# Kernel tuning notes

Measured on AMD Instinct MI355X. Metric: run time of the kernel, lower is better.

## Reference

```python
import jax, jax.numpy as jnp
import numpy as np

H8, W8 = 64, 64
H4, W4 = 128, 128
C_LAT, C_HI = 256, 128
N_Q = 1024
ORIG_H, ORIG_W = 512, 512
NUM_ITERS = 4
TEMP = 20.0
DIM = 4 + C_HI + C_LAT        # 388 mixer output dim
IN_DIM = DIM + 3 * 49         # 535 mixer input dim
HID = 512


def _unit(v):
    return v / jnp.sqrt(jnp.maximum(jnp.sum(v * v, axis=-1, keepdims=True), 1e-12))


def setup_inputs() -> dict:
    key = jax.random.key(0)
    ks = jax.random.split(key, 20)
    fg = _unit(jax.random.normal(ks[0], (1, H8, W8, C_LAT), jnp.float32))
    hg = _unit(jax.random.normal(ks[1], (1, H4, W4, C_HI), jnp.float32))
    qf = _unit(jax.random.normal(ks[2], (1, N_Q, C_LAT), jnp.float32))
    hq = _unit(jax.random.normal(ks[3], (1, N_Q, C_HI), jnp.float32))
    p = lambda k, s, sc=0.05: sc * jax.random.normal(k, s, jnp.float32)
    return dict(
        feature_grid=fg, hires_feats_grid=hg, query_feats=qf, hires_query_feats=hq,
        hid1_w=p(ks[4], (16, 1, 3, 3)), hid1_b=jnp.zeros((16,), jnp.float32),
        hid2_w=p(ks[5], (1, 16, 3, 3)), hid2_b=jnp.zeros((1,), jnp.float32),
        hid3_w=p(ks[6], (32, 16, 3, 3)), hid3_b=jnp.zeros((32,), jnp.float32),
        hid4_w=p(ks[7], (32, 16)), hid4_b=jnp.zeros((16,), jnp.float32),
        occ_w=p(ks[8], (16, 2)), occ_b=jnp.zeros((2,), jnp.float32),
        mix_in_w=p(ks[9], (IN_DIM, HID), 0.02), mix_in_b=jnp.zeros((HID,), jnp.float32),
        mix_out_w=p(ks[10], (HID, DIM), 0.02), mix_out_b=jnp.zeros((DIM,), jnp.float32),
    )


def _conv2d(x, w, b, stride, pad):
    y = jax.lax.conv_general_dilated(x, w, (stride, stride), pad,
                                     dimension_numbers=('NCHW', 'OIHW', 'NCHW'))
    return y + b[None, :, None, None]


def _bilinear_sample(grid, coords):
    # grid [H,W,C]; coords [..., 2] as (y, x); edge-clamped bilinear gather.
    H, W = grid.shape[0], grid.shape[1]
    y, x = coords[..., 0], coords[..., 1]
    y0f, x0f = jnp.floor(y), jnp.floor(x)
    wy, wx = (y - y0f)[..., None], (x - x0f)[..., None]
    y0 = jnp.clip(y0f.astype(jnp.int32), 0, H - 1)
    y1 = jnp.clip(y0f.astype(jnp.int32) + 1, 0, H - 1)
    x0 = jnp.clip(x0f.astype(jnp.int32), 0, W - 1)
    x1 = jnp.clip(x0f.astype(jnp.int32) + 1, 0, W - 1)
    g00, g01 = grid[y0, x0], grid[y0, x1]
    g10, g11 = grid[y1, x0], grid[y1, x1]
    return (g00 * (1 - wy) * (1 - wx) + g01 * (1 - wy) * wx
            + g10 * wy * (1 - wx) + g11 * wy * wx)


def _forward(fg, hg, qf, hq, hid1_w, hid1_b, hid2_w, hid2_b, hid3_w, hid3_b,
             hid4_w, hid4_b, occ_w, occ_b, mix_in_w, mix_in_b, mix_out_w, mix_out_b):
    # --- tracks_from_cost_volume ---
    cv = jnp.einsum('bnc,bhwc->bnhw', qf, fg)                 # [1,N,64,64]
    b, n, h, w = cv.shape
    x = cv.reshape(b * n, 1, h, w)
    occ_map = jax.nn.relu(_conv2d(x, hid1_w, hid1_b, 1, 'SAME'))   # [bn,16,h,w]
    pmap = _conv2d(occ_map, hid2_w, hid2_b, 1, 'SAME').reshape(b * n, h * w)
    heat = jax.nn.softmax(pmap * TEMP, axis=-1).reshape(b * n, h, w)
    ey = jnp.einsum('bhw,h->b', heat, jnp.arange(h, dtype=jnp.float32))
    ex = jnp.einsum('bhw,w->b', heat, jnp.arange(w, dtype=jnp.float32))
    points = jnp.stack([ex * (ORIG_W / w), ey * (ORIG_H / h)], -1).reshape(b, n, 2)
    op = jnp.pad(occ_map, ((0, 0), (0, 0), (0, 2), (0, 2)))
    o3 = jax.nn.relu(_conv2d(op, hid3_w, hid3_b, 2, 'VALID'))
    o3 = o3.mean((-1, -2))                                     # [bn,32]
    o3 = jax.nn.relu(o3 @ hid4_w + hid4_b)
    o3 = (o3 @ occ_w + occ_b).reshape(b, n, 2)
    occ, expd = o3[..., 0], o3[..., 1]

    # --- iterative pips refinement ---
    cy, cx = jnp.meshgrid(jnp.arange(-3, 4), jnp.arange(-3, 4), indexing='ij')
    ctx = jnp.stack([cy, cx], -1).reshape(-1, 2).astype(jnp.float32)   # [49,2] (dy,dx)
    fg_avg = fg.reshape(1, H8 // 2, 2, W8 // 2, 2, C_LAT).mean((2, 4))
    pyramid = [hg, fg, fg_avg]
    feats = jnp.concatenate([hq, qf], -1)                      # [1,N,384]
    pos = points
    for it in range(NUM_ITERS):
        if it == 0:
            queries = [hq[0], qf[0], qf[0]]
        else:
            queries = [feats[0, :, :C_HI], feats[0, :, C_HI:], feats[0, :, C_HI:]]
        corrs = []
        for grid, q in zip(pyramid, queries):
            gh, gw = grid.shape[1], grid.shape[2]
            scale = jnp.array([gw / ORIG_W, gh / ORIG_H], jnp.float32)
            c = (pos[0] * scale)[:, ::-1]                      # (x,y)->(y,x), [N,2]
            coords2 = c[:, None, :] + ctx[None]                # [N,49,2]
            nb = _bilinear_sample(grid[0], coords2)            # [N,49,C]
            corrs.append(jnp.einsum('nsc,nc->ns', nb, q))
        corrs = jnp.concatenate(corrs, -1)[None]               # [1,N,147]
        mlp_in = jnp.concatenate([jnp.zeros_like(pos), occ[..., None],
                                  expd[..., None], feats, corrs], -1)
        res = jax.nn.gelu(mlp_in @ mix_in_w + mix_in_b) @ mix_out_w + mix_out_b
        pos = pos + res[..., :2]
        occ = occ + res[..., 2]
        expd = expd + res[..., 3]
        feats = feats + res[..., 4:]
    return jnp.concatenate([pos, occ[..., None], expd[..., None]], -1)  # [1,N,4]


def reference(feature_grid, hires_feats_grid, query_feats, hires_query_feats,
              hid1_w, hid1_b, hid2_w, hid2_b, hid3_w, hid3_b, hid4_w, hid4_b,
              occ_w, occ_b, mix_in_w, mix_in_b, mix_out_w, mix_out_b):
    return _forward(feature_grid, hires_feats_grid, query_feats, hires_query_feats,
                    hid1_w, hid1_b, hid2_w, hid2_b, hid3_w, hid3_b, hid4_w, hid4_b,
                    occ_w, occ_b, mix_in_w, mix_in_b, mix_out_w, mix_out_b)
```

## Files before the change

kernel.cpp:

```cpp
#include <hip/hip_runtime.h>
#include <hip/hip_bf16.h>
#include <math.h>


#define NQ 1024
#define TEMPF 20.0f
#define DIMV 388
#define INDIM 535
#define KPAD 544
#define HID 512

#define WS_CVB     0
#define WS_WIT     2097152
#define WS_WOT     2236416
#define WS_FG16    2351104
#define WS_HG16    2875392
#define WS_AV16    3923968
#define WS_FGAVG   4194304
#define WS_POS     (WS_FGAVG + 262144)
#define WS_OCC     (WS_POS + NQ*2)
#define WS_EXPD    (WS_OCC + NQ)
#define WS_FEATS   (WS_EXPD + NQ)
#define WS_MLPIN   (WS_FEATS + NQ*384)
#define WS_HIDDEN  (WS_MLPIN + NQ*KPAD)
#define WS_W3B     (WS_HIDDEN + NQ*HID)
#define WS_PART    (WS_MLPIN + 278528)
#define WS_SUM3    WS_HIDDEN

#define CVP 68
#define ROWP 2368

typedef __attribute__((ext_vector_type(8))) short bf16x8;
typedef __attribute__((ext_vector_type(4))) float f32x4;

union BU8 { uint4 u; __hip_bfloat16 h[8]; };

__device__ __forceinline__ int occ_off(int r, int idx, int c) {
  int o = idx * 32 + c * 2;
  o ^= ((idx >> 2) & 3) << 4;
  return r * ROWP + o;
}

__global__ __launch_bounds__(256) void k_prep_cv(
    const float* __restrict__ fg, const float* __restrict__ qf,
    const float* __restrict__ hq, const float* __restrict__ w3,
    float* __restrict__ ws) {
  __shared__ __hip_bfloat16 A_s[32 * 32];
  __shared__ __hip_bfloat16 B_s[64 * 32];
  const int bx = blockIdx.x;
  const int t = threadIdx.x;

  if (bx >= 2048) {
    int i = (bx - 2048) * 256 + t;
    if (i < 262144) {
      int c = i & 255, ox = (i >> 8) & 31, oy = i >> 13;
      const float* b = fg + (((oy * 2) * 64 + ox * 2) << 8) + c;
      ws[WS_FGAVG + i] = 0.25f * (b[0] + b[256] + b[16384] + b[16384 + 256]);
    } else if (i < 262144 + 393216) {
      int j = i - 262144;
      int n = j / 384, c = j - n * 384;
      float v = (c < 128) ? hq[n * 128 + c] : qf[n * 256 + c - 128];
      ws[WS_FEATS + j] = v;
      __hip_bfloat16* mi = (__hip_bfloat16*)(ws + WS_MLPIN);
      mi[n * KPAD + 4 + c] = __float2bfloat16(v);
      if (c == 0) {
        mi[n * KPAD + 0] = __float2bfloat16(0.f);
        mi[n * KPAD + 1] = __float2bfloat16(0.f);
      }
    } else if (i < 262144 + 393216 + 5120) {
      int j = i - (262144 + 393216);
      int e = j & 7, qd = (j >> 3) & 3, nl = (j >> 5) & 15;
      int nt = (j >> 9) & 1, kt = j >> 10;
      int k = kt * 32 + qd * 8 + e;
      int ic = k & 15, tap = k >> 4;
      int oc = nt * 16 + nl;
      float v = (tap < 9) ? w3[(oc * 16 + ic) * 9 + tap] : 0.f;
      ((__hip_bfloat16*)(ws + WS_W3B))[j] = __float2bfloat16(v);
    } else if (i < 262144 + 393216 + 5120 + 524288) {
      int j = i - (262144 + 393216 + 5120);
      ws[WS_SUM3 + j] = 0.f;
    }
    return;
  }

  const int wv = t >> 6, lane = t & 63;
  const int wm = wv & 1, wn = wv >> 1;
  const int quad = lane >> 4, nl = lane & 15;
  const int p0 = (bx & 63) * 64, m0 = (bx >> 6) * 32;
  f32x4 acc0 = {0.f, 0.f, 0.f, 0.f};
  f32x4 acc1 = {0.f, 0.f, 0.f, 0.f};

  for (int k0 = 0; k0 < 256; k0 += 32) {
    {
      int r = t >> 3, c = t & 7;
      float4 v = *(const float4*)&qf[(m0 + r) * 256 + k0 + c * 4];
      union { __hip_bfloat16 h[4]; uint2 u; } pk;
      pk.h[0] = __float2bfloat16(v.x); pk.h[1] = __float2bfloat16(v.y);
      pk.h[2] = __float2bfloat16(v.z); pk.h[3] = __float2bfloat16(v.w);
      *(uint2*)&A_s[r * 32 + c * 4] = pk.u;
    }
    {
      int r = t >> 2, c = t & 3;
      const float* src = &fg[(p0 + r) * 256 + k0 + c * 8];
      float4 v0 = *(const float4*)src;
      float4 v1 = *(const float4*)(src + 4);
      union { __hip_bfloat16 h[8]; uint4 u; } pk;
      pk.h[0] = __float2bfloat16(v0.x); pk.h[1] = __float2bfloat16(v0.y);
      pk.h[2] = __float2bfloat16(v0.z); pk.h[3] = __float2bfloat16(v0.w);
      pk.h[4] = __float2bfloat16(v1.x); pk.h[5] = __float2bfloat16(v1.y);
      pk.h[6] = __float2bfloat16(v1.z); pk.h[7] = __float2bfloat16(v1.w);
      *(uint4*)&B_s[r * 32 + c * 8] = pk.u;
    }
    __syncthreads();
    bf16x8 a = *(const bf16x8*)&A_s[(16 * wm + nl) * 32 + quad * 8];
    bf16x8 b0 = *(const bf16x8*)&B_s[(32 * wn + nl) * 32 + quad * 8];
    bf16x8 b1 = *(const bf16x8*)&B_s[(32 * wn + 16 + nl) * 32 + quad * 8];
    acc0 = __builtin_amdgcn_mfma_f32_16x16x32_bf16(a, b0, acc0, 0, 0, 0);
    acc1 = __builtin_amdgcn_mfma_f32_16x16x32_bf16(a, b1, acc1, 0, 0, 0);
    __syncthreads();
  }
  __hip_bfloat16* cvb = (__hip_bfloat16*)ws;
#pragma unroll
  for (int nt = 0; nt < 2; nt++) {
    int n = p0 + 32 * wn + nt * 16 + nl;
#pragma unroll
    for (int r = 0; r < 4; r++) {
      int m = m0 + 16 * wm + quad * 4 + r;
      cvb[m * 4096 + n] = __float2bfloat16(nt ? acc1[r] : acc0[r]);
    }
  }
}

template <int R>
__device__ __forceinline__ void row_step(
    const float* __restrict__ cvs, int x, int y0, char* occ_t, int chg,
    const float (&w1r)[4][9], const float (&b1r)[4], const float (&w2r)[4][9],
    float (&win)[3][3], float (&pm)[4][3]) {
  if constexpr (R > 0) {
#pragma unroll
    for (int c = 0; c < 3; c++) { win[0][c] = win[1][c]; win[1][c] = win[2][c]; }
    const float* cp = &cvs[(R + 2) * CVP + x];
    win[2][0] = cp[0]; win[2][1] = cp[1]; win[2][2] = cp[2];
  }
  const int yo = y0 - 1 + R;
  if (yo >= 0 && yo <= 63) {
    union { __hip_bfloat16 h[4]; uint2 u; } pk;
#pragma unroll
    for (int k = 0; k < 4; k++) {
      float a = b1r[k];
#pragma unroll
      for (int ky = 0; ky < 3; ky++)
        a += w1r[k][3 * ky] * win[ky][0] + w1r[k][3 * ky + 1] * win[ky][1] +
             w1r[k][3 * ky + 2] * win[ky][2];
      a = fmaxf(a, 0.f);
      pk.h[k] = __float2bfloat16(a);
#pragma unroll
      for (int ky = 0; ky < 3; ky++) {
        if (R - ky >= 0 && R - ky <= 3) {
          pm[R - ky][2] += a * w2r[k][3 * ky + 0];
          pm[R - ky][1] += a * w2r[k][3 * ky + 1];
          pm[R - ky][0] += a * w2r[k][3 * ky + 2];
        }
      }
    }
    *(uint2*)(occ_t + occ_off(R, x + 4, chg)) = pk.u;
  }
}

__global__ __launch_bounds__(256) void k_head_stripe(
    const float* __restrict__ h1w, const float* __restrict__ h1b,
    const float* __restrict__ h2w, const float* __restrict__ h2b,
    const float* __restrict__ h3b, float* __restrict__ ws) {
  __shared__ float cvs[8 * CVP];
  __shared__ float4 occ_t4[6 * ROWP / 16];
  __shared__ float pmbuf[4][4][64];
  char* occ_t = (char*)occ_t4;

  const int bx = blockIdx.x;
  const int q = bx >> 4, st = bx & 15;
  const int y0 = st * 4;
  const int t = threadIdx.x;
  const int wv = t >> 6, lane = t & 63;
  const __hip_bfloat16* cvb = (const __hip_bfloat16*)ws + q * 4096;

  if (t < 192) {
    int r = t >> 5, j = t & 31;
    int off = r * ROWP + ((j < 16) ? j * 8 : 2176 + (j - 16) * 8);
    *(uint2*)(occ_t + off) = make_uint2(0u, 0u);
  }
  if (st == 0 || st == 15) {
    int r = (st == 0) ? 0 : 5;
    for (int i = t; i < 288; i += 256)
      *(uint2*)(occ_t + r * ROWP + i * 8) = make_uint2(0u, 0u);
  }
#pragma unroll
  for (int j = 0; j < 2; j++) {
    int i = t + 256 * j;
    int lr = i >> 6, x = i & 63;
    int g = y0 - 2 + lr;
    cvs[lr * CVP + x + 1] =
        (g >= 0 && g < 64) ? __bfloat162float(cvb[g * 64 + x]) : 0.f;
  }
  if (t < 32) {
    int rr = t >> 2, c = t & 3;
    cvs[rr * CVP + ((c == 0) ? 0 : (64 + c))] = 0.f;
  }
  __syncthreads();

  const int x = lane;
  const int chg = wv * 4;
  float pm[4][3] = {{0.f, 0.f, 0.f}, {0.f, 0.f, 0.f},
                    {0.f, 0.f, 0.f}, {0.f, 0.f, 0.f}};
  {
    float w1r[4][9], b1r[4], w2r[4][9];
#pragma unroll
    for (int k = 0; k < 4; k++) {
      b1r[k] = h1b[chg + k];
#pragma unroll
      for (int j = 0; j < 9; j++) {
        w1r[k][j] = h1w[(chg + k) * 9 + j];
        w2r[k][j] = h2w[(chg + k) * 9 + j];
      }
    }
    float win[3][3];
#pragma unroll
    for (int j = 0; j < 3; j++) {
      const float* cp = &cvs[j * CVP + x];
      win[j][0] = cp[0]; win[j][1] = cp[1]; win[j][2] = cp[2];
    }
    row_step<0>(cvs, x, y0, occ_t, chg, w1r, b1r, w2r, win, pm);
    row_step<1>(cvs, x, y0, occ_t, chg, w1r, b1r, w2r, win, pm);
    row_step<2>(cvs, x, y0, occ_t, chg, w1r, b1r, w2r, win, pm);
    row_step<3>(cvs, x, y0, occ_t, chg, w1r, b1r, w2r, win, pm);
    row_step<4>(cvs, x, y0, occ_t, chg, w1r, b1r, w2r, win, pm);
    row_step<5>(cvs, x, y0, occ_t, chg, w1r, b1r, w2r, win, pm);
  }
#pragma unroll
  for (int pr = 0; pr < 4; pr++) {
    float lf = __shfl(pm[pr][2], lane - 1);
    float rt = __shfl(pm[pr][0], lane + 1);
    if (lane == 0) lf = 0.f;
    if (lane == 63) rt = 0.f;
    pmbuf[wv][pr][x] = pm[pr][1] + lf + rt;
  }
  __syncthreads();

  const int nl = lane & 15;
  const int qd = lane >> 4, qh = qd >> 1, ql = qd & 1;

  if (wv == 1 || wv == 2) {
    const __hip_bfloat16* W3B = (const __hip_bfloat16*)(ws + WS_W3B);
    const int oyl = wv - 1;
    f32x4 acc00 = {0.f, 0.f, 0.f, 0.f}, acc01 = {0.f, 0.f, 0.f, 0.f};
    f32x4 acc10 = {0.f, 0.f, 0.f, 0.f}, acc11 = {0.f, 0.f, 0.f, 0.f};
#pragma unroll
    for (int kt = 0; kt < 5; kt++) {
      int tap = kt * 2 + qh;
      bf16x8 a0, a1;
      if (tap < 9) {
        int ky = (tap >= 6) ? 2 : ((tap >= 3) ? 1 : 0);
        int kx = tap - 3 * ky;
        int R = 2 * oyl + 1 + ky;
        int idx0 = 4 + kx + 2 * nl;
        a0 = *(const bf16x8*)(occ_t + occ_off(R, idx0, ql * 8));
        a1 = *(const bf16x8*)(occ_t + occ_off(R, idx0 + 32, ql * 8));
      } else {
        a0 = (bf16x8){0, 0, 0, 0, 0, 0, 0, 0};
        a1 = a0;
      }
      bf16x8 b0 = *(const bf16x8*)&W3B[((kt * 2 + 0) * 16 + nl) * 32 + qd * 8];
      bf16x8 b1 = *(const bf16x8*)&W3B[((kt * 2 + 1) * 16 + nl) * 32 + qd * 8];
      acc00 = __builtin_amdgcn_mfma_f32_16x16x32_bf16(a0, b0, acc00, 0, 0, 0);
      acc01 = __builtin_amdgcn_mfma_f32_16x16x32_bf16(a0, b1, acc01, 0, 0, 0);
      acc10 = __builtin_amdgcn_mfma_f32_16x16x32_bf16(a1, b0, acc10, 0, 0, 0);
      acc11 = __builtin_amdgcn_mfma_f32_16x16x32_bf16(a1, b1, acc11, 0, 0, 0);
    }
    float bb0 = h3b[nl], bb1 = h3b[16 + nl];
    float s0 = 0.f, s1 = 0.f;
#pragma unroll
    for (int r = 0; r < 4; r++) {
      s0 += fmaxf(acc00[r] + bb0, 0.f) + fmaxf(acc10[r] + bb0, 0.f);
      s1 += fmaxf(acc01[r] + bb1, 0.f) + fmaxf(acc11[r] + bb1, 0.f);
    }
    s0 += __shfl_xor(s0, 16); s0 += __shfl_xor(s0, 32);
    s1 += __shfl_xor(s1, 16); s1 += __shfl_xor(s1, 32);
    if (lane < 16) {
      atomicAdd(&ws[WS_SUM3 + (q * 16 + st) * 32 + nl], s0);
      atomicAdd(&ws[WS_SUM3 + (q * 16 + st) * 32 + 16 + nl], s1);
    }
  } else {
    const int rl = ((wv == 3) ? 2 : 0) + (lane >> 5);
    const int x0 = (lane & 31) * 2;
    float sa = 0.f, sb = 0.f;
#pragma unroll
    for (int w = 0; w < 4; w++) {
      float2 v = *(const float2*)&pmbuf[w][rl][x0];
      sa += v.x; sb += v.y;
    }
    float bb = h2b[0];
    float v0 = (sa + bb) * TEMPF, v1 = (sb + bb) * TEMPF;
    float mg = fmaxf(v0, v1);
#pragma unroll
    for (int off = 1; off < 64; off <<= 1) mg = fmaxf(mg, __shfl_xor(mg, off));
    float e0 = __expf(v0 - mg), e1 = __expf(v1 - mg);
    float s = e0 + e1;
    float sx = e0 * (float)x0 + e1 * (float)(x0 + 1);
    float sy = s * (float)(y0 + rl);
#pragma unroll
    for (int off = 1; off < 64; off <<= 1) {
      s += __shfl_xor(s, off);
      sx += __shfl_xor(sx, off);
      sy += __shfl_xor(sy, off);
    }
    if (lane == 0) {
      int slot = q * 32 + st * 2 + ((wv == 3) ? 1 : 0);
      *(float4*)&ws[WS_PART + slot * 4] = make_float4(mg, s, sx, sy);
    }
  }
}

__global__ __launch_bounds__(256) void k_merge_cvt(
    const float* __restrict__ w4, const float* __restrict__ b4,
    const float* __restrict__ w5, const float* __restrict__ b5,
    const float* __restrict__ wi, const float* __restrict__ wo,
    const float* __restrict__ fg, const float* __restrict__ hg,
    float* __restrict__ ws) {
  {
    int i = blockIdx.x * 256 + threadIdx.x;
    __hip_bfloat16* WIT = (__hip_bfloat16*)(ws + WS_WIT);
    __hip_bfloat16* WOT = (__hip_bfloat16*)(ws + WS_WOT);
    if (i < 278528) {
      int n = i / KPAD, k = i - n * KPAD;
      float v = (k < INDIM) ? wi[k * HID + n] : 0.f;
      WIT[i] = __float2bfloat16(v);
    } else if (i < 507904) {
      int j = i - 278528;
      int n = j >> 9, k = j & 511;
      float v = (n < DIMV) ? wo[k * DIMV + n] : 0.f;
      WOT[j] = __float2bfloat16(v);
    } else {
      int j = i - 507904;
      if (j < 1048576) {
        ((__hip_bfloat16*)(ws + WS_FG16))[j] = __float2bfloat16(fg[j]);
      } else if (j < 3145728) {
        int k = j - 1048576;
        ((__hip_bfloat16*)(ws + WS_HG16))[k] = __float2bfloat16(hg[k]);
      } else if (j < 3407872) {
        int k = j - 3145728;
        ((__hip_bfloat16*)(ws + WS_AV16))[k] = __float2bfloat16(ws[WS_FGAVG + k]);
      }
    }
  }
  if (blockIdx.x >= 256) return;

  __shared__ float sums_s[4][32];
  __shared__ float o4s[4][16];
  int t = threadIdx.x, wv = t >> 6, lane = t & 63;
  int q = blockIdx.x * 4 + wv;

  float M = -1e30f, S = 0.f, SX = 0.f, SY = 0.f;
  if (lane < 32) {
    float4 pv = *(const float4*)&ws[WS_PART + (q * 32 + lane) * 4];
    M = pv.x; S = pv.y; SX = pv.z; SY = pv.w;
  }
#pragma unroll
  for (int off = 1; off < 64; off <<= 1) {
    float Mo = __shfl_xor(M, off), So = __shfl_xor(S, off);
    float SXo = __shfl_xor(SX, off), SYo = __shfl_xor(SY, off);
    float Mn = fmaxf(M, Mo);
    float c1 = __expf(M - Mn), c2 = __expf(Mo - Mn);
    S = S * c1 + So * c2; SX = SX * c1 + SXo * c2; SY = SY * c1 + SYo * c2;
    M = Mn;
  }
  if (lane == 0) {
    ws[WS_POS + q * 2 + 0] = (SX / S) * 8.0f;
    ws[WS_POS + q * 2 + 1] = (SY / S) * 8.0f;
  }

  int ch = lane & 31, half = lane >> 5;
  float sm = 0.f;
#pragma unroll
  for (int s8 = 0; s8 < 8; s8++)
    sm += ws[WS_SUM3 + (q * 16 + half * 8 + s8) * 32 + ch];
  sm += __shfl_xor(sm, 32);
  if (lane < 32) sums_s[wv][lane] = sm * (1.f / 1024.f);
  __syncthreads();
  if (lane < 16) {
    float a = b4[lane];
#pragma unroll
    for (int i = 0; i < 32; i++) a += sums_s[wv][i] * w4[i * 16 + lane];
    o4s[wv][lane] = fmaxf(a, 0.f);
  }
  __syncthreads();
  if (lane < 2) {
    float r = b5[lane];
#pragma unroll
    for (int j = 0; j < 16; j++) r += o4s[wv][j] * w5[j * 2 + lane];
    __hip_bfloat16* mi = (__hip_bfloat16*)(ws + WS_MLPIN);
    if (lane == 0) { ws[WS_OCC + q] = r;  mi[q * KPAD + 2] = __float2bfloat16(r); }
    else           { ws[WS_EXPD + q] = r; mi[q * KPAD + 3] = __float2bfloat16(r); }
  }
}

__global__ __launch_bounds__(256) void k_corr(float* __restrict__ ws) {
  __shared__ float qs[384];
  __shared__ float dbuf[3][64];
  int t = threadIdx.x;
  int wv = t >> 6, lane = t & 63;
  int cl = lane & 15, sub = lane >> 4;
  int n = blockIdx.x;
  const float* feats = ws + WS_FEATS + n * 384;
  float posx = ws[WS_POS + n * 2 + 0];
  float posy = ws[WS_POS + n * 2 + 1];
  __hip_bfloat16* mi = (__hip_bfloat16*)(ws + WS_MLPIN) + n * KPAD;

  for (int col = t; col < 384; col += 256) qs[col] = feats[col];
  __syncthreads();

  float qh[8], qq[16];
#pragma unroll
  for (int j = 0; j < 8; j++) qh[j] = qs[cl * 8 + j];
#pragma unroll
  for (int j = 0; j < 16; j++) qq[j] = qs[128 + cl * 16 + j];

  const __hip_bfloat16* G0 = (const __hip_bfloat16*)(ws + WS_HG16);
  const __hip_bfloat16* G1 = (const __hip_bfloat16*)(ws + WS_FG16);
  const __hip_bfloat16* G2 = (const __hip_bfloat16*)(ws + WS_AV16);

#pragma unroll
  for (int L = 0; L < 3; L++) {
    const __hip_bfloat16* grid;
    int Hg, Wg;
    float scl;
    if (L == 0)      { grid = G0; Hg = 128; Wg = 128; scl = 0.25f; }
    else if (L == 1) { grid = G1; Hg = 64;  Wg = 64;  scl = 0.125f; }
    else             { grid = G2; Hg = 32;  Wg = 32;  scl = 0.0625f; }
    float cy = posy * scl, cx = posx * scl;
    int iy = (int)floorf(cy), ix = (int)floorf(cx);
#pragma unroll
    for (int g = 0; g < 4; g++) {
      int p = wv * 16 + g * 4 + sub;
      int a = p >> 3, b = p & 7;
      int row = iy + a - 3; row = row < 0 ? 0 : (row > Hg - 1 ? Hg - 1 : row);
      int col = ix + b - 3; col = col < 0 ? 0 : (col > Wg - 1 ? Wg - 1 : col);
      float acc = 0.f;
      if (L == 0) {
        BU8 g0; g0.u = *(const uint4*)(grid + (row * Wg + col) * 128 + cl * 8);
#pragma unroll
        for (int j = 0; j < 8; j++) acc += __bfloat162float(g0.h[j]) * qh[j];
      } else {
        const __hip_bfloat16* gp = grid + (row * Wg + col) * 256 + cl * 16;
        BU8 g0, g1;
        g0.u = *(const uint4*)gp;
        g1.u = *(const uint4*)(gp + 8);
#pragma unroll
        for (int j = 0; j < 8; j++) {
          acc += __bfloat162float(g0.h[j]) * qq[j];
          acc += __bfloat162float(g1.h[j]) * qq[8 + j];
        }
      }
      acc += __shfl_xor(acc, 1);
      acc += __shfl_xor(acc, 2);
      acc += __shfl_xor(acc, 4);
      acc += __shfl_xor(acc, 8);
      if (cl == 0) dbuf[L][p] = acc;
    }
  }
  __syncthreads();

  if (t < 147) {
    int L = t / 49, s = t - L * 49;
    int sa = s / 7, sb = s - sa * 7;
    float scl = (L == 0) ? 0.25f : ((L == 1) ? 0.125f : 0.0625f);
    float cy = posy * scl, cx = posx * scl;
    float wy = cy - floorf(cy), wx = cx - floorf(cx);
    int i00 = sa * 8 + sb;
    float d00 = dbuf[L][i00], d01 = dbuf[L][i00 + 1];
    float d10 = dbuf[L][i00 + 8], d11 = dbuf[L][i00 + 9];
    float corr = (1.f - wy) * (1.f - wx) * d00 + (1.f - wy) * wx * d01 +
                 wy * (1.f - wx) * d10 + wy * wx * d11;
    mi[388 + t] = __float2bfloat16(corr);
  }
}

__device__ __forceinline__ float gelu_tanh(float x) {
  float z = 0.7978845608028654f * (x + 0.044715f * x * x * x);
  z = fminf(fmaxf(z, -15.f), 15.f);
  float e = __expf(2.f * z);
  float th = (e - 1.f) / (e + 1.f);
  return 0.5f * x * (1.f + th);
}

__global__ __launch_bounds__(256) void k_mix1(
    const float* __restrict__ bias, float* __restrict__ ws) {
  __shared__ __hip_bfloat16 A_s[32 * 32];
  __shared__ __hip_bfloat16 B_s[32 * 32];
  const int t = threadIdx.x;
  const int wv = t >> 6, lane = t & 63;
  const int wm = wv & 1, wn = wv >> 1;
  const int quad = lane >> 4, nl = lane & 15;
  const int n0 = blockIdx.x * 32, m0 = blockIdx.y * 32;
  const unsigned short* Abf = (const unsigned short*)(ws + WS_MLPIN);
  const unsigned short* WIT = (const unsigned short*)(ws + WS_WIT);
  f32x4 acc = {0.f, 0.f, 0.f, 0.f};

  for (int k0 = 0; k0 < KPAD; k0 += 32) {
    if (t < 128) {
      int r = t >> 2, c = t & 3;
      *(uint4*)&A_s[r * 32 + c * 8] =
          *(const uint4*)&Abf[(m0 + r) * KPAD + k0 + c * 8];
    } else {
      int tt = t - 128;
      int r = tt >> 2, c = tt & 3;
      *(uint4*)&B_s[r * 32 + c * 8] =
          *(const uint4*)&WIT[(n0 + r) * KPAD + k0 + c * 8];
    }
    __syncthreads();
    bf16x8 a = *(const bf16x8*)&A_s[(16 * wm + nl) * 32 + quad * 8];
    bf16x8 b = *(const bf16x8*)&B_s[(16 * wn + nl) * 32 + quad * 8];
    acc = __builtin_amdgcn_mfma_f32_16x16x32_bf16(a, b, acc, 0, 0, 0);
    __syncthreads();
  }

  __hip_bfloat16* Hd = (__hip_bfloat16*)(ws + WS_HIDDEN);
  int nn = n0 + 16 * wn + nl;
  float bv = bias[nn];
#pragma unroll
  for (int r = 0; r < 4; r++) {
    int m = m0 + 16 * wm + quad * 4 + r;
    Hd[m * HID + nn] = __float2bfloat16(gelu_tanh(acc[r] + bv));
  }
}

__global__ __launch_bounds__(256) void k_mix2(
    const float* __restrict__ bias, float* __restrict__ ws,
    float* __restrict__ out) {
  __shared__ __hip_bfloat16 A_s[32 * 32];
  __shared__ __hip_bfloat16 B_s[32 * 32];
  const int t = threadIdx.x;
  const int wv = t >> 6, lane = t & 63;
  const int wm = wv & 1, wn = wv >> 1;
  const int quad = lane >> 4, nl = lane & 15;
  const int n0 = blockIdx.x * 32, m0 = blockIdx.y * 32;
  const unsigned short* Abf = (const unsigned short*)(ws + WS_HIDDEN);
  const unsigned short* WOT = (const unsigned short*)(ws + WS_WOT);
  f32x4 acc = {0.f, 0.f, 0.f, 0.f};

  for (int k0 = 0; k0 < HID; k0 += 32) {
    if (t < 128) {
      int r = t >> 2, c = t & 3;
      *(uint4*)&A_s[r * 32 + c * 8] =
          *(const uint4*)&Abf[(m0 + r) * HID + k0 + c * 8];
    } else {
      int tt = t - 128;
      int r = tt >> 2, c = tt & 3;
      *(uint4*)&B_s[r * 32 + c * 8] =
          *(const uint4*)&WOT[(n0 + r) * HID + k0 + c * 8];
    }
    __syncthreads();
    bf16x8 a = *(const bf16x8*)&A_s[(16 * wm + nl) * 32 + quad * 8];
    bf16x8 b = *(const bf16x8*)&B_s[(16 * wn + nl) * 32 + quad * 8];
    acc = __builtin_amdgcn_mfma_f32_16x16x32_bf16(a, b, acc, 0, 0, 0);
    __syncthreads();
  }

  int col = n0 + 16 * wn + nl;
  if (col < DIMV) {
    float bv = bias[col];
    __hip_bfloat16* mib = (__hip_bfloat16*)(ws + WS_MLPIN);
#pragma unroll
    for (int r = 0; r < 4; r++) {
      int m = m0 + 16 * wm + quad * 4 + r;
      float rr = acc[r] + bv;
      if (col < 2) {
        float v = ws[WS_POS + m * 2 + col] + rr;
        ws[WS_POS + m * 2 + col] = v;
        out[m * 4 + col] = v;
      } else if (col == 2) {
        float v = ws[WS_OCC + m] + rr;
        ws[WS_OCC + m] = v;
        out[m * 4 + 2] = v;
        mib[m * KPAD + 2] = __float2bfloat16(v);
      } else if (col == 3) {
        float v = ws[WS_EXPD + m] + rr;
        ws[WS_EXPD + m] = v;
        out[m * 4 + 3] = v;
        mib[m * KPAD + 3] = __float2bfloat16(v);
      } else {
        float v = ws[WS_FEATS + m * 384 + (col - 4)] + rr;
        ws[WS_FEATS + m * 384 + (col - 4)] = v;
        mib[m * KPAD + col] = __float2bfloat16(v);
      }
    }
  }
}

extern "C" void kernel_launch(void* const* d_in, const int* in_sizes, int n_in,
                              void* d_out, int out_size, void* d_ws, size_t ws_size,
                              hipStream_t stream) {
  const float* fg = (const float*)d_in[0];
  const float* hg = (const float*)d_in[1];
  const float* qf = (const float*)d_in[2];
  const float* hq = (const float*)d_in[3];
  const float* w1 = (const float*)d_in[4];
  const float* b1 = (const float*)d_in[5];
  const float* w2 = (const float*)d_in[6];
  const float* b2 = (const float*)d_in[7];
  const float* w3 = (const float*)d_in[8];
  const float* b3 = (const float*)d_in[9];
  const float* w4 = (const float*)d_in[10];
  const float* b4 = (const float*)d_in[11];
  const float* w5 = (const float*)d_in[12];
  const float* b5 = (const float*)d_in[13];
  const float* wi = (const float*)d_in[14];
  const float* bi = (const float*)d_in[15];
  const float* wo = (const float*)d_in[16];
  const float* bo = (const float*)d_in[17];
  float* ws = (float*)d_ws;
  float* out = (float*)d_out;

  k_prep_cv<<<6676, 256, 0, stream>>>(fg, qf, hq, w3, ws);
  k_head_stripe<<<16384, 256, 0, stream>>>(w1, b1, w2, b2, b3, ws);
  k_merge_cvt<<<15296, 256, 0, stream>>>(w4, b4, w5, b5, wi, wo, fg, hg, ws);
  for (int it = 0; it < 4; it++) {
    k_corr<<<1024, 256, 0, stream>>>(ws);
    k_mix1<<<dim3(16, 32), 256, 0, stream>>>(bi, ws);
    k_mix2<<<dim3(13, 32), 256, 0, stream>>>(bo, ws, out);
  }
}
```

Measured before the change: 370.2 us.

## Fuse per-query head stripes and merge into one block-per-query kernel

The head conv stack previously ran as 16 stripe blocks per query, with atomic partial sums and softmax partials written to workspace and then reduced by a separate merge kernel. Now one 512-thread block per query loops over all 16 stripes. It keeps the whole bf16 cost-volume plane and the conv3 weights in shared memory, accumulates the conv3 sums and an online softmax in registers, and computes the final pos/occ/expd heads in-block. This removes the atomics, the zero-init of the sum buffer, the partial-result round-trips and one reduction kernel. The cost is fewer blocks (1024) with serialized stripes and larger shared-memory use per block.

```diff
diff --git a/kernel.cpp b/kernel.cpp
--- a/kernel.cpp
+++ b/kernel.cpp
@@ -24,10 +24,7 @@
 #define WS_MLPIN   (WS_FEATS + NQ*384)
 #define WS_HIDDEN  (WS_MLPIN + NQ*KPAD)
 #define WS_W3B     (WS_HIDDEN + NQ*HID)
-#define WS_PART    (WS_MLPIN + 278528)
-#define WS_SUM3    WS_HIDDEN
-
-#define CVP 68
+
 #define ROWP 2368
 
 typedef __attribute__((ext_vector_type(8))) short bf16x8;
@@ -67,7 +64,7 @@
         mi[n * KPAD + 0] = __float2bfloat16(0.f);
         mi[n * KPAD + 1] = __float2bfloat16(0.f);
       }
-    } else if (i < 262144 + 393216 + 5120) {
+    } else {
       int j = i - (262144 + 393216);
       int e = j & 7, qd = (j >> 3) & 3, nl = (j >> 5) & 15;
       int nt = (j >> 9) & 1, kt = j >> 10;
@@ -76,9 +73,6 @@
       int oc = nt * 16 + nl;
       float v = (tap < 9) ? w3[(oc * 16 + ic) * 9 + tap] : 0.f;
       ((__hip_bfloat16*)(ws + WS_W3B))[j] = __float2bfloat16(v);
-    } else if (i < 262144 + 393216 + 5120 + 524288) {
-      int j = i - (262144 + 393216 + 5120);
-      ws[WS_SUM3 + j] = 0.f;
     }
     return;
   }
@@ -132,21 +126,23 @@
 }
 
 template <int R>
-__device__ __forceinline__ void row_step(
-    const float* __restrict__ cvs, int x, int y0, char* occ_t, int chg,
-    const float (&w1r)[4][9], const float (&b1r)[4], const float (&w2r)[4][9],
-    float (&win)[3][3], float (&pm)[4][3]) {
+__device__ __forceinline__ void row_step2(
+    const __hip_bfloat16* __restrict__ cvs, int x, int y0, char* occ_t,
+    int chg, const float (&w1r)[2][9], const float (&b1r)[2],
+    const float (&w2r)[2][9], float (&win)[3][3], float (&pm)[4][3]) {
   if constexpr (R > 0) {
 #pragma unroll
     for (int c = 0; c < 3; c++) { win[0][c] = win[1][c]; win[1][c] = win[2][c]; }
-    const float* cp = &cvs[(R + 2) * CVP + x];
-    win[2][0] = cp[0]; win[2][1] = cp[1]; win[2][2] = cp[2];
+    const __hip_bfloat16* cp = &cvs[(y0 + R + 2) * 68 + x + 1];
+    win[2][0] = __bfloat162float(cp[0]);
+    win[2][1] = __bfloat162float(cp[1]);
+    win[2][2] = __bfloat162float(cp[2]);
   }
   const int yo = y0 - 1 + R;
   if (yo >= 0 && yo <= 63) {
-    union { __hip_bfloat16 h[4]; uint2 u; } pk;
-#pragma unroll
-    for (int k = 0; k < 4; k++) {
+    union { __hip_bfloat16 h[2]; uint u; } pk;
+#pragma unroll
+    for (int k = 0; k < 2; k++) {
       float a = b1r[k];
 #pragma unroll
       for (int ky = 0; ky < 3; ky++)
@@ -163,242 +159,227 @@
         }
       }
     }
-    *(uint2*)(occ_t + occ_off(R, x + 4, chg)) = pk.u;
-  }
-}
-
-__global__ __launch_bounds__(256) void k_head_stripe(
+    *(uint*)(occ_t + occ_off(R, x + 4, chg)) = pk.u;
+  }
+}
+
+__global__ __launch_bounds__(512, 4) void k_head(
     const float* __restrict__ h1w, const float* __restrict__ h1b,
     const float* __restrict__ h2w, const float* __restrict__ h2b,
-    const float* __restrict__ h3b, float* __restrict__ ws) {
-  __shared__ float cvs[8 * CVP];
+    const float* __restrict__ h3b, const float* __restrict__ w4,
+    const float* __restrict__ b4, const float* __restrict__ w5,
+    const float* __restrict__ b5, float* __restrict__ ws) {
+  __shared__ __align__(16) __hip_bfloat16 cvs[68 * 68];
   __shared__ float4 occ_t4[6 * ROWP / 16];
-  __shared__ float pmbuf[4][4][64];
+  __shared__ float pmbuf[8][4][64];
+  __shared__ __align__(16) __hip_bfloat16 w3s[5120];
+  __shared__ __align__(16) float red[136];
   char* occ_t = (char*)occ_t4;
 
-  const int bx = blockIdx.x;
-  const int q = bx >> 4, st = bx & 15;
-  const int y0 = st * 4;
+  const int q = blockIdx.x;
   const int t = threadIdx.x;
   const int wv = t >> 6, lane = t & 63;
-  const __hip_bfloat16* cvb = (const __hip_bfloat16*)ws + q * 4096;
-
+  const int x = lane;
+  const int chg = wv * 2;
+
+  for (int i = t; i < 2312; i += 512) ((uint*)cvs)[i] = 0u;
+  {
+    const uint4* src = (const uint4*)(ws + WS_W3B);
+    for (int i = t; i < 640; i += 512) ((uint4*)w3s)[i] = src[i];
+  }
   if (t < 192) {
     int r = t >> 5, j = t & 31;
     int off = r * ROWP + ((j < 16) ? j * 8 : 2176 + (j - 16) * 8);
     *(uint2*)(occ_t + off) = make_uint2(0u, 0u);
   }
-  if (st == 0 || st == 15) {
-    int r = (st == 0) ? 0 : 5;
-    for (int i = t; i < 288; i += 256)
-      *(uint2*)(occ_t + r * ROWP + i * 8) = make_uint2(0u, 0u);
-  }
-#pragma unroll
-  for (int j = 0; j < 2; j++) {
-    int i = t + 256 * j;
-    int lr = i >> 6, x = i & 63;
-    int g = y0 - 2 + lr;
-    cvs[lr * CVP + x + 1] =
-        (g >= 0 && g < 64) ? __bfloat162float(cvb[g * 64 + x]) : 0.f;
-  }
-  if (t < 32) {
-    int rr = t >> 2, c = t & 3;
-    cvs[rr * CVP + ((c == 0) ? 0 : (64 + c))] = 0.f;
-  }
   __syncthreads();
-
-  const int x = lane;
-  const int chg = wv * 4;
-  float pm[4][3] = {{0.f, 0.f, 0.f}, {0.f, 0.f, 0.f},
-                    {0.f, 0.f, 0.f}, {0.f, 0.f, 0.f}};
   {
-    float w1r[4][9], b1r[4], w2r[4][9];
-#pragma unroll
-    for (int k = 0; k < 4; k++) {
-      b1r[k] = h1b[chg + k];
-#pragma unroll
-      for (int j = 0; j < 9; j++) {
-        w1r[k][j] = h1w[(chg + k) * 9 + j];
-        w2r[k][j] = h2w[(chg + k) * 9 + j];
+    const __hip_bfloat16* cvb = (const __hip_bfloat16*)ws + q * 4096;
+    int y = t >> 3, c8 = (t & 7) * 8;
+    uint4 v = *(const uint4*)(cvb + y * 64 + c8);
+    uint* dst = (uint*)&cvs[(y + 2) * 68 + c8 + 2];
+    dst[0] = v.x; dst[1] = v.y; dst[2] = v.z; dst[3] = v.w;
+  }
+
+  float w1r[2][9], w2r[2][9], b1r[2];
+#pragma unroll
+  for (int k = 0; k < 2; k++) {
+    b1r[k] = h1b[chg + k];
+#pragma unroll
+    for (int j = 0; j < 9; j++) {
+      w1r[k][j] = h1w[(chg + k) * 9 + j];
+      w2r[k][j] = h2w[(chg + k) * 9 + j];
+    }
+  }
+  const float bb2 = h2b[0];
+
+  const int nl = lane & 15, qd = lane >> 4, qh = qd >> 1, ql = qd & 1;
+  const bool is_h3 = (wv == 1 || wv == 2 || wv == 5 || wv == 6);
+  const bool is_sm = (wv == 0 || wv == 4);
+  const int oyl = (wv == 2 || wv == 6) ? 1 : 0;
+  const int mh = (wv >= 4) ? 1 : 0;
+  const int smrl = ((wv == 4) ? 2 : 0) + (lane >> 5);
+  const int x0 = (lane & 31) * 2;
+  const float bb0 = h3b[nl], bb1 = h3b[16 + nl];
+  float s0a = 0.f, s1a = 0.f;
+  float M = -1e30f, S = 0.f, SX = 0.f, SY = 0.f;
+  __syncthreads();
+
+  for (int st = 0; st < 16; st++) {
+    const int y0 = st * 4;
+    if (st == 15 && t < 296)
+      *(uint2*)(occ_t + 5 * ROWP + t * 8) = make_uint2(0u, 0u);
+
+    float pm[4][3] = {{0.f, 0.f, 0.f}, {0.f, 0.f, 0.f},
+                      {0.f, 0.f, 0.f}, {0.f, 0.f, 0.f}};
+    float win[3][3];
+#pragma unroll
+    for (int j = 0; j < 3; j++) {
+      const __hip_bfloat16* cp = &cvs[(y0 + j) * 68 + x + 1];
+      win[j][0] = __bfloat162float(cp[0]);
+      win[j][1] = __bfloat162float(cp[1]);
+      win[j][2] = __bfloat162float(cp[2]);
+    }
+    row_step2<0>(cvs, x, y0, occ_t, chg, w1r, b1r, w2r, win, pm);
+    row_step2<1>(cvs, x, y0, occ_t, chg, w1r, b1r, w2r, win, pm);
+    row_step2<2>(cvs, x, y0, occ_t, chg, w1r, b1r, w2r, win, pm);
+    row_step2<3>(cvs, x, y0, occ_t, chg, w1r, b1r, w2r, win, pm);
+    row_step2<4>(cvs, x, y0, occ_t, chg, w1r, b1r, w2r, win, pm);
+    row_step2<5>(cvs, x, y0, occ_t, chg, w1r, b1r, w2r, win, pm);
+#pragma unroll
+    for (int pr = 0; pr < 4; pr++) {
+      float lf = __shfl(pm[pr][2], lane - 1);
+      float rt = __shfl(pm[pr][0], lane + 1);
+      if (lane == 0) lf = 0.f;
+      if (lane == 63) rt = 0.f;
+      pmbuf[wv][pr][x] = pm[pr][1] + lf + rt;
+    }
+    __syncthreads();
+
+    if (is_h3) {
+      f32x4 acc0 = {0.f, 0.f, 0.f, 0.f}, acc1 = {0.f, 0.f, 0.f, 0.f};
+#pragma unroll
+      for (int kt = 0; kt < 5; kt++) {
+        int tap = kt * 2 + qh;
+        bf16x8 a;
+        if (tap < 9) {
+          int ky = (tap >= 6) ? 2 : ((tap >= 3) ? 1 : 0);
+          int kx = tap - 3 * ky;
+          a = *(const bf16x8*)(occ_t +
+              occ_off(2 * oyl + 1 + ky, 4 + kx + 2 * nl + 32 * mh, ql * 8));
+        } else {
+          a = (bf16x8){0, 0, 0, 0, 0, 0, 0, 0};
+        }
+        bf16x8 b0 = *(const bf16x8*)&w3s[((kt * 2 + 0) * 16 + nl) * 32 + qd * 8];
+        bf16x8 b1 = *(const bf16x8*)&w3s[((kt * 2 + 1) * 16 + nl) * 32 + qd * 8];
+        acc0 = __builtin_amdgcn_mfma_f32_16x16x32_bf16(a, b0, acc0, 0, 0, 0);
+        acc1 = __builtin_amdgcn_mfma_f32_16x16x32_bf16(a, b1, acc1, 0, 0, 0);
       }
-    }
-    float win[3][3];
-#pragma unroll
-    for (int j = 0; j < 3; j++) {
-      const float* cp = &cvs[j * CVP + x];
-      win[j][0] = cp[0]; win[j][1] = cp[1]; win[j][2] = cp[2];
-    }
-    row_step<0>(cvs, x, y0, occ_t, chg, w1r, b1r, w2r, win, pm);
-    row_step<1>(cvs, x, y0, occ_t, chg, w1r, b1r, w2r, win, pm);
-    row_step<2>(cvs, x, y0, occ_t, chg, w1r, b1r, w2r, win, pm);
-    row_step<3>(cvs, x, y0, occ_t, chg, w1r, b1r, w2r, win, pm);
-    row_step<4>(cvs, x, y0, occ_t, chg, w1r, b1r, w2r, win, pm);
-    row_step<5>(cvs, x, y0, occ_t, chg, w1r, b1r, w2r, win, pm);
-  }
-#pragma unroll
-  for (int pr = 0; pr < 4; pr++) {
-    float lf = __shfl(pm[pr][2], lane - 1);
-    float rt = __shfl(pm[pr][0], lane + 1);
-    if (lane == 0) lf = 0.f;
-    if (lane == 63) rt = 0.f;
-    pmbuf[wv][pr][x] = pm[pr][1] + lf + rt;
+#pragma unroll
+      for (int r = 0; r < 4; r++) {
+        s0a += fmaxf(acc0[r] + bb0, 0.f);
+        s1a += fmaxf(acc1[r] + bb1, 0.f);
+      }
+    } else if (is_sm) {
+      float sa = 0.f, sb = 0.f;
+#pragma unroll
+      for (int w = 0; w < 8; w++) {
+        float2 v = *(const float2*)&pmbuf[w][smrl][x0];
+        sa += v.x; sb += v.y;
+      }
+      float v0 = (sa + bb2) * TEMPF, v1 = (sb + bb2) * TEMPF;
+      float Mn = fmaxf(M, fmaxf(v0, v1));
+      float c = __expf(M - Mn);
+      float e0 = __expf(v0 - Mn), e1 = __expf(v1 - Mn);
+      S = S * c + e0 + e1;
+      SX = SX * c + e0 * (float)x0 + e1 * (float)(x0 + 1);
+      SY = SY * c + (e0 + e1) * (float)(y0 + smrl);
+      M = Mn;
+    }
+    __syncthreads();
+  }
+
+  if (is_h3) {
+    s0a += __shfl_xor(s0a, 16); s0a += __shfl_xor(s0a, 32);
+    s1a += __shfl_xor(s1a, 16); s1a += __shfl_xor(s1a, 32);
+    int slot = oyl * 2 + mh;
+    if (lane < 16) {
+      red[slot * 32 + nl] = s0a;
+      red[slot * 32 + 16 + nl] = s1a;
+    }
+  }
+  if (is_sm) {
+#pragma unroll
+    for (int off = 1; off < 64; off <<= 1) {
+      float Mo = __shfl_xor(M, off), So = __shfl_xor(S, off);
+      float SXo = __shfl_xor(SX, off), SYo = __shfl_xor(SY, off);
+      float Mn = fmaxf(M, Mo);
+      float c1 = __expf(M - Mn), c2 = __expf(Mo - Mn);
+      S = S * c1 + So * c2; SX = SX * c1 + SXo * c2; SY = SY * c1 + SYo * c2;
+      M = Mn;
+    }
+    if (lane == 0)
+      *(float4*)&red[128 + (wv >> 2) * 4] = make_float4(M, S, SX, SY);
   }
   __syncthreads();
 
-  const int nl = lane & 15;
-  const int qd = lane >> 4, qh = qd >> 1, ql = qd & 1;
-
-  if (wv == 1 || wv == 2) {
-    const __hip_bfloat16* W3B = (const __hip_bfloat16*)(ws + WS_W3B);
-    const int oyl = wv - 1;
-    f32x4 acc00 = {0.f, 0.f, 0.f, 0.f}, acc01 = {0.f, 0.f, 0.f, 0.f};
-    f32x4 acc10 = {0.f, 0.f, 0.f, 0.f}, acc11 = {0.f, 0.f, 0.f, 0.f};
-#pragma unroll
-    for (int kt = 0; kt < 5; kt++) {
-      int tap = kt * 2 + qh;
-      bf16x8 a0, a1;
-      if (tap < 9) {
-        int ky = (tap >= 6) ? 2 : ((tap >= 3) ? 1 : 0);
-        int kx = tap - 3 * ky;
-        int R = 2 * oyl + 1 + ky;
-        int idx0 = 4 + kx + 2 * nl;
-        a0 = *(const bf16x8*)(occ_t + occ_off(R, idx0, ql * 8));
-        a1 = *(const bf16x8*)(occ_t + occ_off(R, idx0 + 32, ql * 8));
-      } else {
-        a0 = (bf16x8){0, 0, 0, 0, 0, 0, 0, 0};
-        a1 = a0;
-      }
-      bf16x8 b0 = *(const bf16x8*)&W3B[((kt * 2 + 0) * 16 + nl) * 32 + qd * 8];
-      bf16x8 b1 = *(const bf16x8*)&W3B[((kt * 2 + 1) * 16 + nl) * 32 + qd * 8];
-      acc00 = __builtin_amdgcn_mfma_f32_16x16x32_bf16(a0, b0, acc00, 0, 0, 0);
-      acc01 = __builtin_amdgcn_mfma_f32_16x16x32_bf16(a0, b1, acc01, 0, 0, 0);
-      acc10 = __builtin_amdgcn_mfma_f32_16x16x32_bf16(a1, b0, acc10, 0, 0, 0);
-      acc11 = __builtin_amdgcn_mfma_f32_16x16x32_bf16(a1, b1, acc11, 0, 0, 0);
-    }
-    float bb0 = h3b[nl], bb1 = h3b[16 + nl];
-    float s0 = 0.f, s1 = 0.f;
-#pragma unroll
-    for (int r = 0; r < 4; r++) {
-      s0 += fmaxf(acc00[r] + bb0, 0.f) + fmaxf(acc10[r] + bb0, 0.f);
-      s1 += fmaxf(acc01[r] + bb1, 0.f) + fmaxf(acc11[r] + bb1, 0.f);
-    }
-    s0 += __shfl_xor(s0, 16); s0 += __shfl_xor(s0, 32);
-    s1 += __shfl_xor(s1, 16); s1 += __shfl_xor(s1, 32);
-    if (lane < 16) {
-      atomicAdd(&ws[WS_SUM3 + (q * 16 + st) * 32 + nl], s0);
-      atomicAdd(&ws[WS_SUM3 + (q * 16 + st) * 32 + 16 + nl], s1);
-    }
-  } else {
-    const int rl = ((wv == 3) ? 2 : 0) + (lane >> 5);
-    const int x0 = (lane & 31) * 2;
-    float sa = 0.f, sb = 0.f;
-#pragma unroll
-    for (int w = 0; w < 4; w++) {
-      float2 v = *(const float2*)&pmbuf[w][rl][x0];
-      sa += v.x; sb += v.y;
-    }
-    float bb = h2b[0];
-    float v0 = (sa + bb) * TEMPF, v1 = (sb + bb) * TEMPF;
-    float mg = fmaxf(v0, v1);
-#pragma unroll
-    for (int off = 1; off < 64; off <<= 1) mg = fmaxf(mg, __shfl_xor(mg, off));
-    float e0 = __expf(v0 - mg), e1 = __expf(v1 - mg);
-    float s = e0 + e1;
-    float sx = e0 * (float)x0 + e1 * (float)(x0 + 1);
-    float sy = s * (float)(y0 + rl);
-#pragma unroll
-    for (int off = 1; off < 64; off <<= 1) {
-      s += __shfl_xor(s, off);
-      sx += __shfl_xor(sx, off);
-      sy += __shfl_xor(sy, off);
-    }
+  if (wv == 0) {
+    float4 Pa = *(const float4*)&red[128];
+    float4 Pb = *(const float4*)&red[132];
+    float Mn = fmaxf(Pa.x, Pb.x);
+    float ca = __expf(Pa.x - Mn), cb = __expf(Pb.x - Mn);
+    float Sf = Pa.y * ca + Pb.y * cb;
+    float SXf = Pa.z * ca + Pb.z * cb;
+    float SYf = Pa.w * ca + Pb.w * cb;
     if (lane == 0) {
-      int slot = q * 32 + st * 2 + ((wv == 3) ? 1 : 0);
-      *(float4*)&ws[WS_PART + slot * 4] = make_float4(mg, s, sx, sy);
-    }
-  }
-}
-
-__global__ __launch_bounds__(256) void k_merge_cvt(
-    const float* __restrict__ w4, const float* __restrict__ b4,
-    const float* __restrict__ w5, const float* __restrict__ b5,
+      ws[WS_POS + q * 2 + 0] = (SXf / Sf) * 8.0f;
+      ws[WS_POS + q * 2 + 1] = (SYf / Sf) * 8.0f;
+    }
+    int l = lane & 15;
+    float a = b4[l];
+#pragma unroll
+    for (int i = 0; i < 32; i++) {
+      float sm = (red[i] + red[32 + i] + red[64 + i] + red[96 + i]) *
+                 (1.f / 1024.f);
+      a += sm * w4[i * 16 + l];
+    }
+    float o4 = fmaxf(a, 0.f);
+    float rr = b5[lane & 1];
+#pragma unroll
+    for (int j = 0; j < 16; j++) rr += __shfl(o4, j) * w5[j * 2 + (lane & 1)];
+    __hip_bfloat16* mi = (__hip_bfloat16*)(ws + WS_MLPIN);
+    if (lane == 0) { ws[WS_OCC + q] = rr;  mi[q * KPAD + 2] = __float2bfloat16(rr); }
+    if (lane == 1) { ws[WS_EXPD + q] = rr; mi[q * KPAD + 3] = __float2bfloat16(rr); }
+  }
+}
+
+__global__ __launch_bounds__(256) void k_cvt(
     const float* __restrict__ wi, const float* __restrict__ wo,
     const float* __restrict__ fg, const float* __restrict__ hg,
     float* __restrict__ ws) {
-  {
-    int i = blockIdx.x * 256 + threadIdx.x;
-    __hip_bfloat16* WIT = (__hip_bfloat16*)(ws + WS_WIT);
-    __hip_bfloat16* WOT = (__hip_bfloat16*)(ws + WS_WOT);
-    if (i < 278528) {
-      int n = i / KPAD, k = i - n * KPAD;
-      float v = (k < INDIM) ? wi[k * HID + n] : 0.f;
-      WIT[i] = __float2bfloat16(v);
-    } else if (i < 507904) {
-      int j = i - 278528;
-      int n = j >> 9, k = j & 511;
-      float v = (n < DIMV) ? wo[k * DIMV + n] : 0.f;
-      WOT[j] = __float2bfloat16(v);
-    } else {
-      int j = i - 507904;
-      if (j < 1048576) {
-        ((__hip_bfloat16*)(ws + WS_FG16))[j] = __float2bfloat16(fg[j]);
-      } else if (j < 3145728) {
-        int k = j - 1048576;
-        ((__hip_bfloat16*)(ws + WS_HG16))[k] = __float2bfloat16(hg[k]);
-      } else if (j < 3407872) {
-        int k = j - 3145728;
-        ((__hip_bfloat16*)(ws + WS_AV16))[k] = __float2bfloat16(ws[WS_FGAVG + k]);
-      }
-    }
-  }
-  if (blockIdx.x >= 256) return;
-
-  __shared__ float sums_s[4][32];
-  __shared__ float o4s[4][16];
-  int t = threadIdx.x, wv = t >> 6, lane = t & 63;
-  int q = blockIdx.x * 4 + wv;
-
-  float M = -1e30f, S = 0.f, SX = 0.f, SY = 0.f;
-  if (lane < 32) {
-    float4 pv = *(const float4*)&ws[WS_PART + (q * 32 + lane) * 4];
-    M = pv.x; S = pv.y; SX = pv.z; SY = pv.w;
-  }
-#pragma unroll
-  for (int off = 1; off < 64; off <<= 1) {
-    float Mo = __shfl_xor(M, off), So = __shfl_xor(S, off);
-    float SXo = __shfl_xor(SX, off), SYo = __shfl_xor(SY, off);
-    float Mn = fmaxf(M, Mo);
-    float c1 = __expf(M - Mn), c2 = __expf(Mo - Mn);
-    S = S * c1 + So * c2; SX = SX * c1 + SXo * c2; SY = SY * c1 + SYo * c2;
-    M = Mn;
-  }
-  if (lane == 0) {
-    ws[WS_POS + q * 2 + 0] = (SX / S) * 8.0f;
-    ws[WS_POS + q * 2 + 1] = (SY / S) * 8.0f;
-  }
-
-  int ch = lane & 31, half = lane >> 5;
-  float sm = 0.f;
-#pragma unroll
-  for (int s8 = 0; s8 < 8; s8++)
-    sm += ws[WS_SUM3 + (q * 16 + half * 8 + s8) * 32 + ch];
-  sm += __shfl_xor(sm, 32);
-  if (lane < 32) sums_s[wv][lane] = sm * (1.f / 1024.f);
-  __syncthreads();
-  if (lane < 16) {
-    float a = b4[lane];
-#pragma unroll
-    for (int i = 0; i < 32; i++) a += sums_s[wv][i] * w4[i * 16 + lane];
-    o4s[wv][lane] = fmaxf(a, 0.f);
-  }
-  __syncthreads();
-  if (lane < 2) {
-    float r = b5[lane];
-#pragma unroll
-    for (int j = 0; j < 16; j++) r += o4s[wv][j] * w5[j * 2 + lane];
-    __hip_bfloat16* mi = (__hip_bfloat16*)(ws + WS_MLPIN);
-    if (lane == 0) { ws[WS_OCC + q] = r;  mi[q * KPAD + 2] = __float2bfloat16(r); }
-    else           { ws[WS_EXPD + q] = r; mi[q * KPAD + 3] = __float2bfloat16(r); }
+  int i = blockIdx.x * 256 + threadIdx.x;
+  __hip_bfloat16* WIT = (__hip_bfloat16*)(ws + WS_WIT);
+  __hip_bfloat16* WOT = (__hip_bfloat16*)(ws + WS_WOT);
+  if (i < 278528) {
+    int n = i / KPAD, k = i - n * KPAD;
+    float v = (k < INDIM) ? wi[k * HID + n] : 0.f;
+    WIT[i] = __float2bfloat16(v);
+  } else if (i < 507904) {
+    int j = i - 278528;
+    int n = j >> 9, k = j & 511;
+    float v = (n < DIMV) ? wo[k * DIMV + n] : 0.f;
+    WOT[j] = __float2bfloat16(v);
+  } else {
+    int j = i - 507904;
+    if (j < 1048576) {
+      ((__hip_bfloat16*)(ws + WS_FG16))[j] = __float2bfloat16(fg[j]);
+    } else if (j < 3145728) {
+      int k = j - 1048576;
+      ((__hip_bfloat16*)(ws + WS_HG16))[k] = __float2bfloat16(hg[k]);
+    } else if (j < 3407872) {
+      int k = j - 3145728;
+      ((__hip_bfloat16*)(ws + WS_AV16))[k] = __float2bfloat16(ws[WS_FGAVG + k]);
+    }
   }
 }
 
@@ -619,9 +600,9 @@
   float* ws = (float*)d_ws;
   float* out = (float*)d_out;
 
-  k_prep_cv<<<6676, 256, 0, stream>>>(fg, qf, hq, w3, ws);
-  k_head_stripe<<<16384, 256, 0, stream>>>(w1, b1, w2, b2, b3, ws);
-  k_merge_cvt<<<15296, 256, 0, stream>>>(w4, b4, w5, b5, wi, wo, fg, hg, ws);
+  k_prep_cv<<<4628, 256, 0, stream>>>(fg, qf, hq, w3, ws);
+  k_head<<<1024, 512, 0, stream>>>(w1, b1, w2, b2, b3, w4, b4, w5, b5, ws);
+  k_cvt<<<15296, 256, 0, stream>>>(wi, wo, fg, hg, ws);
   for (int it = 0; it < 4; it++) {
     k_corr<<<1024, 256, 0, stream>>>(ws);
     k_mix1<<<dim3(16, 32), 256, 0, stream>>>(bi, ws);
```

New measurement: 382.2 us. +3.3%, slower.
